# Optimization experiments

Measured on AMD Instinct MI355X. Metric: run time of the kernel, lower is better.

Reference implementation:

```python
import jax, jax.numpy as jnp
import numpy as np

EPS_RMS = 1.1920929e-07  # torch.finfo(float32).eps (nn.RMSNorm default eps=None)
EPS_LN = 1e-5
SCALE = 64 ** -0.5       # Attention.scale uses default dim_head=64, NOT dim_head_qk
SOFTCLAMP = 5.0
DEPTH = 4
H, DQK, DV = 8, 128, 192
D, DP = 768, 128
SEQ, NPAIR, B = 2048, 256, 1
FF_INNER = int(D * 2.0)
DP_INNER = int(DP * 2.0)
MAX_POS = 8192


def rmsnorm(x, w):
    return x * jax.lax.rsqrt(jnp.mean(x * x, axis=-1, keepdims=True) + EPS_RMS) * w


def layernorm_nb(x, w):  # LayerNorm(bias=False)
    mu = jnp.mean(x, axis=-1, keepdims=True)
    var = jnp.mean((x - mu) ** 2, axis=-1, keepdims=True)
    return (x - mu) * jax.lax.rsqrt(var + EPS_LN) * w


def rotate_half(x):
    x1, x2 = jnp.split(x, 2, axis=-1)
    return jnp.concatenate((-x2, x1), axis=-1)


def apply_rotary(pos, t):
    return t * jnp.cos(pos) + rotate_half(t) * jnp.sin(pos)


def rotary_table(seq_len):
    # faithful to source: inv_freq = 1/(arange(nf) + logspace(1, max_pos-nf+1, nf))
    nf = DQK // 2
    inv_freq = 1.0 / (jnp.arange(nf, dtype=jnp.float32)
                      + 10.0 ** jnp.linspace(1.0, float(MAX_POS - nf + 1), nf, dtype=jnp.float32))
    freqs = jnp.arange(seq_len, dtype=jnp.float32)[:, None] * inv_freq  # [n, nf]
    return jnp.concatenate((freqs, freqs), axis=-1)  # [n, DQK]


def softclamp(t):
    return jnp.tanh(t / SOFTCLAMP) * SOFTCLAMP


def _forward(single, pairwise, attn_pre_w, attn_post_w, qkv_w, q_norm_w, k_norm_w,
             v_norm_w, bias_rms_w, bias_proj_w, out_w, ff_pre_w, ff_post_w,
             ff_w1, ff_b1, ff_w2, ff_b2, pw_attn_pre_w, pw_qk_w, pw_v_w, pw_v_b,
             pw_ff_pre_w, pw_ff_w1, pw_ff_b1, pw_ff_w2, pw_ff_b2):
    b, n, _ = single.shape
    pos = rotary_table(n)
    pw_idx = 0
    for i in range(DEPTH):
        # ---- attention block (sandwich RMSNorm) ----
        res = single
        xn = rmsnorm(single, attn_pre_w[i])
        qkv = xn @ qkv_w[i]
        q, k, v = jnp.split(qkv, [H * DQK, H * DQK + DQK], axis=-1)
        q = q.reshape(b, n, H, DQK).transpose(0, 2, 1, 3)  # b h n d (k,v are single-head)
        q = layernorm_nb(q, q_norm_w[i]) * SCALE
        k = layernorm_nb(k, k_norm_w[i])
        v = layernorm_nb(v, v_norm_w[i])
        q = apply_rotary(pos, q)
        k = apply_rotary(pos, k)
        sim = jnp.einsum('bhid,bjd->bhij', q, k)
        # pairwise bias: RMSNorm -> GELU -> Linear(dp, heads) -> b h i j, nearest-repeat to seq
        pb = jax.nn.gelu(rmsnorm(pairwise, bias_rms_w[i]), approximate=False) @ bias_proj_w[i]
        pb = pb.transpose(0, 3, 1, 2)  # b h i j
        r = sim.shape[-1] // pb.shape[-1]
        pb = jnp.repeat(jnp.repeat(pb, r, axis=2), r, axis=3)
        attn = jax.nn.softmax(softclamp(sim + pb), axis=-1)
        out = jnp.einsum('bhij,bjd->bhid', attn, v)
        out = out.transpose(0, 2, 1, 3).reshape(b, n, H * DV)
        single = rmsnorm(out @ out_w[i], attn_post_w[i]) + res
        # ---- feedforward (sandwich RMSNorm) ----
        res = single
        xn = rmsnorm(single, ff_pre_w[i])
        h = jax.nn.relu(xn @ ff_w1[i] + ff_b1[i])
        single = rmsnorm(h @ ff_w2[i] + ff_b2[i], ff_post_w[i]) + res
        # ---- pairwise track every other layer (no sandwich) ----
        if i % 2 == 0:
            j = pw_idx
            res = pairwise
            xn = rmsnorm(pairwise, pw_attn_pre_w[j])
            pq, pk = jnp.split(xn @ pw_qk_w[j], 2, axis=-1)
            pv = xn @ pw_v_w[j] + pw_v_b[j]
            psim = jnp.einsum('bnid,bnjd->bnij', pq, pk)  # source never applies its scale
            pairwise = jnp.einsum('bnij,bnjd->bnid', jax.nn.softmax(psim, axis=-1), pv) + res
            res = pairwise
            xn = rmsnorm(pairwise, pw_ff_pre_w[j])
            hh = jax.nn.relu(xn @ pw_ff_w1[j] + pw_ff_b1[j])
            pairwise = hh @ pw_ff_w2[j] + pw_ff_b2[j] + res
            pw_idx += 1
    return single, pairwise


def setup_inputs() -> dict:
    key = jax.random.key(0)
    ks = iter(jax.random.split(key, 40))
    nrm = lambda shape: jax.random.normal(next(ks), shape, jnp.float32) * 0.02
    n_pw = (DEPTH + 1) // 2
    return dict(
        single=jax.random.normal(next(ks), (B, SEQ, D), jnp.float32),
        pairwise=jax.random.normal(next(ks), (B, NPAIR, NPAIR, DP), jnp.float32),
        attn_pre_w=jnp.ones((DEPTH, D), jnp.float32),
        attn_post_w=jnp.ones((DEPTH, D), jnp.float32),
        qkv_w=nrm((DEPTH, D, H * DQK + DQK + DV)),
        q_norm_w=jnp.ones((DEPTH, DQK), jnp.float32),
        k_norm_w=jnp.ones((DEPTH, DQK), jnp.float32),
        v_norm_w=jnp.ones((DEPTH, DV), jnp.float32),
        bias_rms_w=jnp.ones((DEPTH, DP), jnp.float32),
        bias_proj_w=nrm((DEPTH, DP, H)),
        out_w=nrm((DEPTH, H * DV, D)),
        ff_pre_w=jnp.ones((DEPTH, D), jnp.float32),
        ff_post_w=jnp.ones((DEPTH, D), jnp.float32),
        ff_w1=nrm((DEPTH, D, FF_INNER)),
        ff_b1=jnp.zeros((DEPTH, FF_INNER), jnp.float32),
        ff_w2=nrm((DEPTH, FF_INNER, D)),
        ff_b2=jnp.zeros((DEPTH, D), jnp.float32),
        pw_attn_pre_w=jnp.ones((n_pw, DP), jnp.float32),
        pw_qk_w=nrm((n_pw, DP, 2 * DP)),
        pw_v_w=nrm((n_pw, DP, DP)),
        pw_v_b=jnp.zeros((n_pw, DP), jnp.float32),
        pw_ff_pre_w=jnp.ones((n_pw, DP), jnp.float32),
        pw_ff_w1=nrm((n_pw, DP, DP_INNER)),
        pw_ff_b1=jnp.zeros((n_pw, DP_INNER), jnp.float32),
        pw_ff_w2=nrm((n_pw, DP_INNER, DP)),
        pw_ff_b2=jnp.zeros((n_pw, DP), jnp.float32),
    )


def reference(single, pairwise, attn_pre_w, attn_post_w, qkv_w, q_norm_w, k_norm_w,
              v_norm_w, bias_rms_w, bias_proj_w, out_w, ff_pre_w, ff_post_w,
              ff_w1, ff_b1, ff_w2, ff_b2, pw_attn_pre_w, pw_qk_w, pw_v_w, pw_v_b,
              pw_ff_pre_w, pw_ff_w1, pw_ff_b1, pw_ff_w2, pw_ff_b2):
    return _forward(single, pairwise, attn_pre_w, attn_post_w, qkv_w, q_norm_w,
                    k_norm_w, v_norm_w, bias_rms_w, bias_proj_w, out_w, ff_pre_w,
                    ff_post_w, ff_w1, ff_b1, ff_w2, ff_b2, pw_attn_pre_w, pw_qk_w,
                    pw_v_w, pw_v_b, pw_ff_pre_w, pw_ff_w1, pw_ff_b1, pw_ff_w2, pw_ff_b2)
```

## Files before the change

### kernel.cpp

```cpp
#include <hip/hip_runtime.h>
#include <hip/hip_bf16.h>

#define SEQ 2048
#define DMODEL 768
#define NHEAD 8
#define DQK 128
#define DV 192
#define QKVN 1344
#define FFI 1536
#define NP 256
#define DP 128
#define DPI 256
#define NPR 65536
#define KVB 64
#define NSPLIT 2

#define EPS_RMS 1.1920929e-07f
#define EPS_LN 1e-5f
#define LOG2E 1.4426950408889634f
#define C1_LOG2E 0.5770780163555852f
#define C2_LOG2E -14.426950408889634f

typedef __attribute__((ext_vector_type(8))) short bf16x8;
typedef __attribute__((ext_vector_type(4))) short bf16x4;
typedef __attribute__((ext_vector_type(4))) float f32x4;

__device__ inline float wave_sum(float v) {
#pragma unroll
  for (int o = 32; o > 0; o >>= 1) v += __shfl_xor(v, o, 64);
  return v;
}
__device__ inline unsigned short f2bf(float x) {
  unsigned int u = __float_as_uint(x);
  u += 0x7fffu + ((u >> 16) & 1u);
  return (unsigned short)(u >> 16);
}
__device__ inline float bf2f(unsigned short x) {
  unsigned int u = ((unsigned int)x) << 16;
  return __uint_as_float(u);
}

__global__ void pos_kernel(float* __restrict__ pos) {
  int i = blockIdx.x, l = threadIdx.x;
  float f = (l == 0) ? 0.1f * (float)i : 0.0f;
  pos[i * 128 + l] = f;
  pos[i * 128 + 64 + l] = f;
}

__global__ void rowscale_kernel(const float* __restrict__ x, float* __restrict__ sc, int cols) {
  size_t row = blockIdx.x;
  int l = threadIdx.x;
  const float* xr = x + row * cols;
  float ss = 0.f;
  for (int c = l; c < cols; c += 64) { float v = xr[c]; ss += v * v; }
  ss = wave_sum(ss);
  if (l == 0) sc[row] = rsqrtf(ss / (float)cols + EPS_RMS);
}

__global__ void rmsres_kernel(const float* __restrict__ x, const float* __restrict__ w,
                              const float* res, float* y, int cols, float* __restrict__ sc) {
  size_t row = blockIdx.x;
  int l = threadIdx.x;
  const float* xr = x + row * cols;
  float ss = 0.f;
  for (int c = l; c < cols; c += 64) { float v = xr[c]; ss += v * v; }
  ss = wave_sum(ss);
  float r = rsqrtf(ss / (float)cols + EPS_RMS);
  float* yr = y + row * cols;
  const float* rr = res + row * cols;
  float ss2 = 0.f;
  for (int c = l; c < cols; c += 64) {
    float v = xr[c] * r * w[c] + rr[c];
    yr[c] = v;
    ss2 += v * v;
  }
  ss2 = wave_sum(ss2);
  if (l == 0) sc[row] = rsqrtf(ss2 / (float)cols + EPS_RMS);
}

struct ConvBatch {
  const float* src[24];
  unsigned short* dst[24];
  int K[24];
  int N[24];
  int base[24];
};

__global__ __launch_bounds__(256) void convT_batch(ConvBatch cb, int nw) {
  __shared__ float ls[32][33];
  int bid = blockIdx.x;
  int w = 0;
  while (w + 1 < nw && bid >= cb.base[w + 1]) w++;
  int local = bid - cb.base[w];
  int K = cb.K[w], N = cb.N[w];
  int ntn = N >> 5;
  int n0 = (local % ntn) * 32, k0 = (local / ntn) * 32;
  const float* W = cb.src[w];
  unsigned short* Wt = cb.dst[w];
  int t = threadIdx.x;
  int c = t & 31, r4 = t >> 5;
#pragma unroll
  for (int p = 0; p < 4; p++) {
    int r = r4 + p * 8;
    ls[r][c] = W[(size_t)(k0 + r) * N + n0 + c];
  }
  __syncthreads();
#pragma unroll
  for (int p = 0; p < 4; p++) {
    int n = r4 + p * 8, k = t & 31;
    Wt[(size_t)(n0 + n) * K + k0 + k] = f2bf(ls[k][n]);
  }
}

__global__ void biasbuild_kernel(const float* __restrict__ pw_v_b, float* __restrict__ b384) {
  int j = blockIdx.x, t = threadIdx.x;
  b384[j * 384 + t] = (t < 256) ? 0.f : pw_v_b[j * DP + t - 256];
}

template<int AMODE, int CBF, int RBF = 0, int BN64 = 0>
__global__ __launch_bounds__(256) void gemm_k(const void* __restrict__ Av,
    const unsigned short* __restrict__ Bt, void* __restrict__ Cv,
    int M, int N, int K, int nbx,
    const float* __restrict__ bias, const void* __restrict__ resid, int act,
    const float* __restrict__ ascale, const float* __restrict__ aw,
    const float* __restrict__ lb = nullptr) {
  constexpr int BN = BN64 ? 64 : 128;
  constexpr int NC = BN64 ? 2 : 4;
  __shared__ unsigned short As[64 * 32];
  __shared__ unsigned short Bs[BN * 32];
  int t = threadIdx.x;
  int nwg = gridDim.x, bid = blockIdx.x;
  int qq = nwg >> 3, rr = nwg & 7, xc = bid & 7, ii = bid >> 3;
  int swz = (xc < rr ? xc * (qq + 1) : rr * (qq + 1) + (xc - rr) * qq) + ii;
  int bm = (swz / nbx) * 64, bn = (swz % nbx) * BN;
  int w = t >> 6, l = t & 63;
  int wr = (w >> 1) * 32, wc = (w & 1) * (BN / 2);
  int lo = l & 15, hi = l >> 4;
  f32x4 acc[2][NC];
#pragma unroll
  for (int q = 0; q < 2; q++)
#pragma unroll
    for (int cb = 0; cb < NC; cb++) acc[q][cb] = (f32x4){0.f, 0.f, 0.f, 0.f};

  int arow = t >> 2, acs = (t & 3) * 8;
  int brow = BN64 ? (t >> 2) : (t >> 1);
  int bks  = BN64 ? ((t & 3) * 8) : ((t & 1) * 16);
  int bok = (bn + brow < N);
  const unsigned short* bsrc = Bt + (size_t)(bok ? bn + brow : 0) * K + bks;

  float4 pa0, pa1;
  bf16x8 pab, pc1, pb0, pb1;
  float linv = 1.f;
  const bf16x8 zb = {0, 0, 0, 0, 0, 0, 0, 0};

  {
    if (AMODE == 2) {
      const unsigned short* Op = (const unsigned short*)Av;
      size_t base = (size_t)(bm + arow) * K + acs;
      pab = *(const bf16x8*)(Op + base);
      pc1 = *(const bf16x8*)(Op + (size_t)SEQ * K + base);
      int h = acs / DV;
      linv = 1.0f / (lb[(size_t)h * SEQ + bm + arow] +
                     lb[(size_t)(NHEAD + h) * SEQ + bm + arow]);
    } else if (AMODE == 1 || AMODE == 3) {
      pab = *(const bf16x8*)((const unsigned short*)Av + (size_t)(bm + arow) * K + acs);
    } else {
      const float* A = (const float*)Av;
      pa0 = *(const float4*)(A + (size_t)(bm + arow) * K + acs);
      pa1 = *(const float4*)(A + (size_t)(bm + arow) * K + acs + 4);
    }
    pb0 = bok ? *(const bf16x8*)(bsrc) : zb;
    if (!BN64) pb1 = bok ? *(const bf16x8*)(bsrc + 8) : zb;
  }

  for (int k0 = 0; k0 < K; k0 += 32) {
    if (k0) __syncthreads();
    {
      int byte = (arow * 64 + acs * 2) ^ ((arow & 7) << 4);
      if (AMODE == 2) {
        bf16x8 cmb;
#pragma unroll
        for (int e = 0; e < 8; e++)
          cmb[e] = (short)f2bf((bf2f((unsigned short)pab[e]) +
                                bf2f((unsigned short)pc1[e])) * linv);
        *(bf16x8*)((char*)As + byte) = cmb;
      } else if (AMODE == 3) {
        float s = ascale[bm + arow];
        bf16x8 sc8;
#pragma unroll
        for (int e = 0; e < 8; e++)
          sc8[e] = (short)f2bf(bf2f((unsigned short)pab[e]) * s * aw[k0 + acs + e]);
        *(bf16x8*)((char*)As + byte) = sc8;
      } else if (AMODE == 1) {
        *(bf16x8*)((char*)As + byte) = pab;
      } else {
        float4 v0 = pa0, v1 = pa1;
        if (ascale) {
          float s = ascale[bm + arow];
          v0.x *= s * aw[k0 + acs + 0]; v0.y *= s * aw[k0 + acs + 1];
          v0.z *= s * aw[k0 + acs + 2]; v0.w *= s * aw[k0 + acs + 3];
          v1.x *= s * aw[k0 + acs + 4]; v1.y *= s * aw[k0 + acs + 5];
          v1.z *= s * aw[k0 + acs + 6]; v1.w *= s * aw[k0 + acs + 7];
        }
        uint4 pk;
        pk.x = (unsigned int)f2bf(v0.x) | ((unsigned int)f2bf(v0.y) << 16);
        pk.y = (unsigned int)f2bf(v0.z) | ((unsigned int)f2bf(v0.w) << 16);
        pk.z = (unsigned int)f2bf(v1.x) | ((unsigned int)f2bf(v1.y) << 16);
        pk.w = (unsigned int)f2bf(v1.z) | ((unsigned int)f2bf(v1.w) << 16);
        *(uint4*)((char*)As + byte) = pk;
      }
      int b0 = (brow * 64 + bks * 2) ^ ((brow & 7) << 4);
      *(bf16x8*)((char*)Bs + b0) = pb0;
      if (!BN64) {
        int b1 = (brow * 64 + bks * 2 + 16) ^ ((brow & 7) << 4);
        *(bf16x8*)((char*)Bs + b1) = pb1;
      }
    }
    __syncthreads();
    if (k0 + 32 < K) {
      int kn = k0 + 32;
      if (AMODE == 2) {
        const unsigned short* Op = (const unsigned short*)Av;
        size_t base = (size_t)(bm + arow) * K + kn + acs;
        pab = *(const bf16x8*)(Op + base);
        pc1 = *(const bf16x8*)(Op + (size_t)SEQ * K + base);
        int h = (kn + acs) / DV;
        linv = 1.0f / (lb[(size_t)h * SEQ + bm + arow] +
                       lb[(size_t)(NHEAD + h) * SEQ + bm + arow]);
      } else if (AMODE == 1 || AMODE == 3) {
        pab = *(const bf16x8*)((const unsigned short*)Av + (size_t)(bm + arow) * K + kn + acs);
      } else {
        const float* A = (const float*)Av;
        pa0 = *(const float4*)(A + (size_t)(bm + arow) * K + kn + acs);
        pa1 = *(const float4*)(A + (size_t)(bm + arow) * K + kn + acs + 4);
      }
      pb0 = bok ? *(const bf16x8*)(bsrc + kn) : zb;
      if (!BN64) pb1 = bok ? *(const bf16x8*)(bsrc + kn + 8) : zb;
    }
    bf16x8 af[2], bfr[NC];
#pragma unroll
    for (int q = 0; q < 2; q++) {
      int r = wr + q * 16 + lo;
      af[q] = *(const bf16x8*)((char*)As + ((r * 64 + hi * 16) ^ ((r & 7) << 4)));
    }
#pragma unroll
    for (int cb = 0; cb < NC; cb++) {
      int n = wc + cb * 16 + lo;
      bfr[cb] = *(const bf16x8*)((char*)Bs + ((n * 64 + hi * 16) ^ ((n & 7) << 4)));
    }
#pragma unroll
    for (int q = 0; q < 2; q++)
#pragma unroll
      for (int cb = 0; cb < NC; cb++)
        acc[q][cb] = __builtin_amdgcn_mfma_f32_16x16x32_bf16(af[q], bfr[cb], acc[q][cb], 0, 0, 0);
  }
#pragma unroll
  for (int q = 0; q < 2; q++) {
#pragma unroll
    for (int cb = 0; cb < NC; cb++) {
      int gn = bn + wc + cb * 16 + lo;
      if (gn >= N) continue;
#pragma unroll
      for (int i = 0; i < 4; i++) {
        int gm = bm + wr + q * 16 + hi * 4 + i;
        float v = acc[q][cb][i];
        if (bias) v += bias[gn];
        if (act) v = fmaxf(v, 0.f);
        if (resid) {
          size_t ridx = (size_t)gm * N + gn;
          v += RBF ? bf2f(((const unsigned short*)resid)[ridx])
                   : ((const float*)resid)[ridx];
        }
        if (CBF) {
          ((unsigned short*)Cv)[(size_t)gm * N + gn] = f2bf(v);
        } else {
          ((float*)Cv)[(size_t)gm * N + gn] = v;
        }
      }
    }
  }
}

__global__ void qkv_prep_kernel(const unsigned short* __restrict__ qkv,
                                const float* __restrict__ qw,
                                const float* __restrict__ kw, const float* __restrict__ vw,
                                const float* __restrict__ pos,
                                unsigned short* __restrict__ q_r, unsigned short* __restrict__ k_n,
                                unsigned short* __restrict__ v_t) {
  int i = blockIdx.x;
  int y = blockIdx.y;
  int l = threadIdx.x;
  if (y == 9) {
    const unsigned short* row = qkv + (size_t)i * QKVN + NHEAD * DQK + DQK;
    float x0 = bf2f(row[l]), x1 = bf2f(row[l + 64]), x2 = bf2f(row[l + 128]);
    float mu = wave_sum(x0 + x1 + x2) * (1.0f / 192.0f);
    float d0 = x0 - mu, d1 = x1 - mu, d2 = x2 - mu;
    float var = wave_sum(d0 * d0 + d1 * d1 + d2 * d2) * (1.0f / 192.0f);
    float rs = rsqrtf(var + EPS_LN);
    v_t[(size_t)l * SEQ + i] = f2bf(d0 * rs * vw[l]);
    v_t[(size_t)(l + 64) * SEQ + i] = f2bf(d1 * rs * vw[l + 64]);
    v_t[(size_t)(l + 128) * SEQ + i] = f2bf(d2 * rs * vw[l + 128]);
    return;
  }
  int off = (y < 8) ? y * DQK : NHEAD * DQK;
  const unsigned short* row = qkv + (size_t)i * QKVN + off;
  float a = bf2f(row[l]), b = bf2f(row[l + 64]);
  float mu = wave_sum(a + b) * (1.0f / 128.0f);
  float da = a - mu, db = b - mu;
  float var = wave_sum(da * da + db * db) * (1.0f / 128.0f);
  float rs = rsqrtf(var + EPS_LN);
  const float* w = (y < 8) ? qw : kw;
  float na = da * rs * w[l], nb = db * rs * w[l + 64];
  if (y < 8) { na *= 0.125f; nb *= 0.125f; }
  float p0 = pos[i * 128 + l], p1 = pos[i * 128 + 64 + l];
  float ra = na * cosf(p0) - nb * sinf(p0);
  float rb = nb * cosf(p1) + na * sinf(p1);
  if (y < 8) {
    unsigned short* o = q_r + ((size_t)y * SEQ + i) * DQK;
    o[l] = f2bf(ra); o[l + 64] = f2bf(rb);
  } else {
    unsigned short* o = k_n + (size_t)i * DQK;
    o[l] = f2bf(ra); o[l + 64] = f2bf(rb);
  }
}

__global__ __launch_bounds__(256) void pb_kernel(const float* __restrict__ P,
    float* __restrict__ scP, const float* __restrict__ rmsw,
    const float* __restrict__ proj, float* __restrict__ pbt) {
  __shared__ float gs[32][130];
  __shared__ float projs[1024];
  int b = blockIdx.x, t = threadIdx.x;
  int row0 = b * 32;
  int wv = t >> 6, ln = t & 63;
  for (int f = t; f < 1024; f += 256) projs[f] = proj[f];
#pragma unroll
  for (int rr = 0; rr < 8; rr++) {
    int r = wv * 8 + rr;
    const float* src = P + (size_t)(row0 + r) * DP;
    float2 x = *(const float2*)(src + ln * 2);
    float ss = wave_sum(x.x * x.x + x.y * x.y);
    float rs = rsqrtf(ss * (1.0f / DP) + EPS_RMS);
    float g0 = x.x * rs * rmsw[ln * 2];
    float g1 = x.y * rs * rmsw[ln * 2 + 1];
    gs[r][ln * 2] = 0.5f * g0 * (1.0f + erff(g0 * 0.70710678118654752f));
    gs[r][ln * 2 + 1] = 0.5f * g1 * (1.0f + erff(g1 * 0.70710678118654752f));
    if (ln == 0) scP[row0 + r] = rs;
  }
  __syncthreads();
  int hh = t >> 5, r = t & 31;
  float acc = 0.f;
#pragma unroll 4
  for (int d = 0; d < 128; d++) acc += gs[r][d] * projs[d * 8 + hh];
  pbt[(size_t)hh * NPR + row0 + r] = acc;
}

__global__ __launch_bounds__(256) void attn_mfma(const unsigned short* __restrict__ q_r,
    const unsigned short* __restrict__ k_n, const unsigned short* __restrict__ v_t,
    const float* __restrict__ pbt, unsigned short* __restrict__ Opart,
    float* __restrict__ lbuf) {
  __shared__ unsigned short Ks[64 * 128];
  __shared__ unsigned short Vs[208 * 64];
  __shared__ unsigned short Ps[4][16 * 64];
  __shared__ float pb_lds[64];
  int ib = blockIdx.x, h = blockIdx.y, sp = blockIdx.z, t = threadIdx.x;
  int i0 = ib * 64;
  int w = t >> 6, l = t & 63;
  int lo = l & 15, hi = l >> 4;
  int kbeg = sp * (SEQ / NSPLIT), kend = kbeg + SEQ / NSPLIT;

  bf16x8 qf[4];
  {
    const unsigned short* qp = q_r + ((size_t)h * SEQ + i0 + w * 16 + lo) * DQK + hi * 8;
#pragma unroll
    for (int ks = 0; ks < 4; ks++) qf[ks] = *(const bf16x8*)(qp + ks * 32);
  }
  f32x4 o_acc[13];
#pragma unroll
  for (int vc = 0; vc < 13; vc++) o_acc[vc] = (f32x4){0.f, 0.f, 0.f, 0.f};

#pragma unroll
  for (int r4 = 0; r4 < 4; r4++) {
    int idx = t + 256 * r4;
    int row = 192 + (idx >> 6), key = idx & 63;
    int byte = (row * 128 + key * 2) ^ ((row & 7) << 4);
    *(unsigned short*)((char*)Vs + byte) = (row == 192) ? 0x3F80 : 0;
  }

  char* PsW = (char*)&Ps[w][0];
  int rg8 = (((w * 16 + lo) >> 3) << 3) + (hi >> 1);

  for (int k0 = kbeg; k0 < kend; k0 += KVB) {
    {
      int row = t >> 2, d0 = (t & 3) * 32;
      const unsigned short* src = k_n + (size_t)(k0 + row) * DQK + d0;
#pragma unroll
      for (int jj = 0; jj < 4; jj++) {
        bf16x8 a = *(const bf16x8*)(src + jj * 8);
        int byte = (row * 256 + (d0 + jj * 8) * 2) ^ ((row & 7) << 4);
        *(bf16x8*)((char*)Ks + byte) = a;
      }
    }
#pragma unroll
    for (int rep = 0; rep < 6; rep++) {
      int c = t + 256 * rep;
      int row = c >> 3, seg = c & 7;
      bf16x8 a = *(const bf16x8*)(v_t + (size_t)row * SEQ + k0 + seg * 8);
      int byte = (row * 128 + seg * 16) ^ ((row & 7) << 4);
      *(bf16x8*)((char*)Vs + byte) = a;
    }
    if (t < 64) {
      int rg = t >> 3, kg = t & 7;
      pb_lds[t] = C1_LOG2E * pbt[(size_t)h * NPR + ((i0 >> 3) + rg) * 256 + (k0 >> 3) + kg];
    }
    __syncthreads();
    f32x4 sacc[4];
#pragma unroll
    for (int kb = 0; kb < 4; kb++) sacc[kb] = (f32x4){0.f, 0.f, 0.f, 0.f};
#pragma unroll
    for (int ks = 0; ks < 4; ks++) {
#pragma unroll
      for (int kb = 0; kb < 4; kb++) {
        int key = kb * 16 + lo;
        int byte = (key * 256 + (ks * 32 + hi * 8) * 2) ^ ((key & 7) << 4);
        bf16x8 kf = *(const bf16x8*)((char*)Ks + byte);
        sacc[kb] = __builtin_amdgcn_mfma_f32_16x16x32_bf16(kf, qf[ks], sacc[kb], 0, 0, 0);
      }
    }
#pragma unroll
    for (int kb = 0; kb < 4; kb++) {
      float pb = pb_lds[rg8 + kb * 2];
      bf16x4 pk;
#pragma unroll
      for (int i = 0; i < 4; i++) {
        float x2 = fmaf(C1_LOG2E, sacc[kb][i], pb);
        float e = __builtin_amdgcn_exp2f(x2);
        float p = __builtin_amdgcn_exp2f(C2_LOG2E * __builtin_amdgcn_rcpf(e + 1.f));
        pk[i] = (short)f2bf(p);
      }
      int byte = (lo * 128 + (kb * 32 + hi * 8)) ^ ((lo & 7) << 4);
      *(bf16x4*)(PsW + byte) = pk;
    }
#pragma unroll
    for (int ks2 = 0; ks2 < 2; ks2++) {
      int byte = (lo * 128 + (ks2 * 32 + hi * 8) * 2) ^ ((lo & 7) << 4);
      bf16x8 pa = *(const bf16x8*)(PsW + byte);
#pragma unroll
      for (int vc = 0; vc < 13; vc++) {
        int dv = vc * 16 + lo;
        int vbyte = (dv * 128 + (ks2 * 32 + hi * 8) * 2) ^ ((dv & 7) << 4);
        bf16x8 bv = *(const bf16x8*)((char*)Vs + vbyte);
        o_acc[vc] = __builtin_amdgcn_mfma_f32_16x16x32_bf16(pa, bv, o_acc[vc], 0, 0, 0);
      }
    }
    __syncthreads();
  }
#pragma unroll
  for (int i = 0; i < 4; i++) {
    int row = i0 + w * 16 + hi * 4 + i;
    unsigned short* orow = Opart + (size_t)sp * SEQ * (NHEAD * DV) +
                           (size_t)row * (NHEAD * DV) + h * DV;
#pragma unroll
    for (int vc = 0; vc < 12; vc++) orow[vc * 16 + lo] = f2bf(o_acc[vc][i]);
    if (lo == 0) lbuf[((size_t)sp * NHEAD + h) * SEQ + row] = o_acc[12][i];
  }
}

__global__ __launch_bounds__(256) void pw_attn_mfma(const unsigned short* __restrict__ pqkv,
    const float* __restrict__ resid, unsigned short* __restrict__ out,
    float* __restrict__ scP) {
  __shared__ unsigned short Ks[64 * 128];
  __shared__ unsigned short Vs[128 * 64];
  __shared__ unsigned short Ps[4][16 * 64];
  int qb = blockIdx.x, nl = blockIdx.y, t = threadIdx.x;
  int i0 = qb * 64;
  int w = t >> 6, l = t & 63;
  int lo = l & 15, hi = l >> 4;
  size_t nrow = (size_t)nl * NP;

  bf16x8 qf[4];
  {
    const unsigned short* qp = pqkv + (nrow + i0 + w * 16 + lo) * 384 + hi * 8;
#pragma unroll
    for (int ks = 0; ks < 4; ks++) qf[ks] = *(const bf16x8*)(qp + ks * 32);
  }
  float m_s[4], l_s[4];
  f32x4 o_acc[8];
#pragma unroll
  for (int i = 0; i < 4; i++) { m_s[i] = -1e30f; l_s[i] = 0.f; }
#pragma unroll
  for (int vc = 0; vc < 8; vc++) o_acc[vc] = (f32x4){0.f, 0.f, 0.f, 0.f};
  char* PsW = (char*)&Ps[w][0];

  for (int k0 = 0; k0 < NP; k0 += 64) {
    {
      int row = t >> 2, d0 = (t & 3) * 32;
      const unsigned short* src = pqkv + (nrow + k0 + row) * 384 + DP + d0;
#pragma unroll
      for (int jj = 0; jj < 4; jj++) {
        bf16x8 a = *(const bf16x8*)(src + jj * 8);
        int byte = (row * 256 + (d0 + jj * 8) * 2) ^ ((row & 7) << 4);
        *(bf16x8*)((char*)Ks + byte) = a;
      }
    }
    {
      int key = t & 63, ds0 = (t >> 6) * 32;
      const unsigned short* src = pqkv + (nrow + k0 + key) * 384 + 256 + ds0;
#pragma unroll
      for (int e = 0; e < 4; e++) {
        bf16x8 a = *(const bf16x8*)(src + e * 8);
#pragma unroll
        for (int e2 = 0; e2 < 8; e2++) {
          int dv = ds0 + e * 8 + e2;
          *(unsigned short*)((char*)Vs + ((dv * 128 + key * 2) ^ ((dv & 7) << 4))) =
              (unsigned short)a[e2];
        }
      }
    }
    __syncthreads();
    f32x4 sacc[4];
#pragma unroll
    for (int cs = 0; cs < 4; cs++) sacc[cs] = (f32x4){0.f, 0.f, 0.f, 0.f};
#pragma unroll
    for (int ks = 0; ks < 4; ks++) {
#pragma unroll
      for (int cs = 0; cs < 4; cs++) {
        int key = cs * 16 + lo;
        int byte = (key * 256 + (ks * 32 + hi * 8) * 2) ^ ((key & 7) << 4);
        bf16x8 bk = *(const bf16x8*)((char*)Ks + byte);
        sacc[cs] = __builtin_amdgcn_mfma_f32_16x16x32_bf16(qf[ks], bk, sacc[cs], 0, 0, 0);
      }
    }
#pragma unroll
    for (int i = 0; i < 4; i++) {
      float mrow = fmaxf(fmaxf(sacc[0][i], sacc[1][i]), fmaxf(sacc[2][i], sacc[3][i]));
#pragma unroll
      for (int ofs = 1; ofs < 16; ofs <<= 1) mrow = fmaxf(mrow, __shfl_xor(mrow, ofs, 64));
      float mn = fmaxf(m_s[i], mrow);
      float mnl = mn * LOG2E;
      float scale = __builtin_amdgcn_exp2f(fmaf(m_s[i], LOG2E, -mnl));
      float ts = 0.f;
      int r = hi * 4 + i;
#pragma unroll
      for (int cs = 0; cs < 4; cs++) {
        float p = __builtin_amdgcn_exp2f(fmaf(sacc[cs][i], LOG2E, -mnl));
        ts += p;
        int key = cs * 16 + lo;
        int byte = (r * 128 + key * 2) ^ ((r & 7) << 4);
        *(unsigned short*)(PsW + byte) = f2bf(p);
      }
#pragma unroll
      for (int ofs = 1; ofs < 16; ofs <<= 1) ts += __shfl_xor(ts, ofs, 64);
      l_s[i] = l_s[i] * scale + ts;
      m_s[i] = mn;
#pragma unroll
      for (int vc = 0; vc < 8; vc++) o_acc[vc][i] *= scale;
    }
#pragma unroll
    for (int ks2 = 0; ks2 < 2; ks2++) {
      int byte = (lo * 128 + (ks2 * 32 + hi * 8) * 2) ^ ((lo & 7) << 4);
      bf16x8 pa = *(const bf16x8*)(PsW + byte);
#pragma unroll
      for (int vc = 0; vc < 8; vc++) {
        int dv = vc * 16 + lo;
        int vbyte = (dv * 128 + (ks2 * 32 + hi * 8) * 2) ^ ((dv & 7) << 4);
        bf16x8 bv = *(const bf16x8*)((char*)Vs + vbyte);
        o_acc[vc] = __builtin_amdgcn_mfma_f32_16x16x32_bf16(pa, bv, o_acc[vc], 0, 0, 0);
      }
    }
    __syncthreads();
  }
#pragma unroll
  for (int i = 0; i < 4; i++) {
    float inv = 1.0f / l_s[i];
    size_t growi = nrow + i0 + w * 16 + hi * 4 + i;
    size_t grow = growi * DP;
    float ss = 0.f;
#pragma unroll
    for (int vc = 0; vc < 8; vc++) {
      int dv = vc * 16 + lo;
      float v = o_acc[vc][i] * inv + resid[grow + dv];
      out[grow + dv] = f2bf(v);
      ss += v * v;
    }
#pragma unroll
    for (int ofs = 1; ofs < 16; ofs <<= 1) ss += __shfl_xor(ss, ofs, 64);
    if (lo == 0) scP[growi] = rsqrtf(ss * (1.0f / DP) + EPS_RMS);
  }
}

extern "C" void kernel_launch(void* const* d_in, const int* in_sizes, int n_in,
                              void* d_out, int out_size, void* d_ws, size_t ws_size,
                              hipStream_t stream) {
  const float* in_single   = (const float*)d_in[0];
  const float* in_pair     = (const float*)d_in[1];
  const float* attn_pre_w  = (const float*)d_in[2];
  const float* attn_post_w = (const float*)d_in[3];
  const float* qkv_w       = (const float*)d_in[4];
  const float* q_norm_w    = (const float*)d_in[5];
  const float* k_norm_w    = (const float*)d_in[6];
  const float* v_norm_w    = (const float*)d_in[7];
  const float* bias_rms_w  = (const float*)d_in[8];
  const float* bias_proj_w = (const float*)d_in[9];
  const float* out_w       = (const float*)d_in[10];
  const float* ff_pre_w    = (const float*)d_in[11];
  const float* ff_post_w   = (const float*)d_in[12];
  const float* ff_w1       = (const float*)d_in[13];
  const float* ff_b1       = (const float*)d_in[14];
  const float* ff_w2       = (const float*)d_in[15];
  const float* ff_b2       = (const float*)d_in[16];
  const float* pw_attn_pre = (const float*)d_in[17];
  const float* pw_qk_w     = (const float*)d_in[18];
  const float* pw_v_w      = (const float*)d_in[19];
  const float* pw_v_b      = (const float*)d_in[20];
  const float* pw_ff_pre   = (const float*)d_in[21];
  const float* pw_ff_w1    = (const float*)d_in[22];
  const float* pw_ff_b1    = (const float*)d_in[23];
  const float* pw_ff_w2    = (const float*)d_in[24];
  const float* pw_ff_b2    = (const float*)d_in[25];

  float* ws = (float*)d_ws;
  float* S    = ws;
  float* Pc   = ws + 1572864;
  float* Pa   = ws + 9961472;
  float* pbt  = ws + 18350080;
  float* pos  = ws + 18874368;
  float* scP  = ws + 19136512;
  float* scS  = ws + 19202048;
  float* TMP  = ws + 19204096;
  unsigned short* qkv_bf = (unsigned short*)TMP;
  unsigned short* q_r_bf = (unsigned short*)(TMP + 2752512);
  unsigned short* k_n_bf = (unsigned short*)(TMP + 3801088);
  unsigned short* v_t_bf = (unsigned short*)(TMP + 3932160);
  float* t2   = TMP + 655360;
  unsigned short* t1_bf = (unsigned short*)(TMP + 2752512);
  unsigned short* Opart = (unsigned short*)Pa;
  float* lbuf = Pa + 6500000;
  unsigned short* Pa_bf = (unsigned short*)Pa;
  float* bias384       = TMP + 6420000;
  unsigned short* Warena = (unsigned short*)(ws + 27854848);
  unsigned short* Wpw = Warena + (size_t)4 * 4571136;
  unsigned short* pqkv_full = (unsigned short*)(ws + 37111808);
  unsigned short* hh_full   = pqkv_full;

  float* outS = (float*)d_out;
  float* outP = outS + (size_t)SEQ * DMODEL;

  pos_kernel<<<SEQ, 64, 0, stream>>>(pos);
  rowscale_kernel<<<SEQ, 64, 0, stream>>>(in_single, scS, DMODEL);
  biasbuild_kernel<<<2, 384, 0, stream>>>(pw_v_b, bias384);

  {
    ConvBatch cb;
    int idx = 0, base = 0;
    auto add = [&](const float* s, unsigned short* d, int K, int N) {
      cb.src[idx] = s; cb.dst[idx] = d; cb.K[idx] = K; cb.N[idx] = N; cb.base[idx] = base;
      base += (N / 32) * (K / 32);
      idx++;
    };
    for (int l = 0; l < 4; l++) {
      unsigned short* WA = Warena + (size_t)l * 4571136;
      add(qkv_w + (size_t)l * DMODEL * QKVN, WA, DMODEL, QKVN);
      add(out_w + (size_t)l * (NHEAD * DV) * DMODEL, WA + 1032192, NHEAD * DV, DMODEL);
      add(ff_w1 + (size_t)l * DMODEL * FFI, WA + 2211840, DMODEL, FFI);
      add(ff_w2 + (size_t)l * FFI * DMODEL, WA + 3391488, FFI, DMODEL);
    }
    for (int j = 0; j < 2; j++) {
      unsigned short* WEF = Wpw + (size_t)j * 114688;
      add(pw_qk_w + (size_t)j * DP * 2 * DP, WEF, DP, 2 * DP);
      add(pw_v_w + (size_t)j * DP * DP, WEF + 256 * DP, DP, DP);
      add(pw_ff_w1 + (size_t)j * DP * DPI, WEF + 49152, DP, DPI);
      add(pw_ff_w2 + (size_t)j * DPI * DP, WEF + 81920, DPI, DP);
    }
    convT_batch<<<base, 256, 0, stream>>>(cb, idx);
  }

  for (int i = 0; i < 4; i++) {
    int j = i / 2;
    unsigned short* WA  = Warena + (size_t)i * 4571136;
    unsigned short* WO  = WA + 1032192;
    unsigned short* WF1 = WA + 2211840;
    unsigned short* WF2 = WA + 3391488;
    unsigned short* WEF = Wpw + (size_t)j * 114688;
    unsigned short* WG  = WEF + 49152;
    unsigned short* WH  = WEF + 81920;

    const float* Psrc = (i == 0) ? in_pair : ((i == 3) ? outP : Pc);
    const float* Ssrc = (i == 0) ? in_single : S;

    pb_kernel<<<2048, 256, 0, stream>>>(Psrc, scP, bias_rms_w + i * DP,
                                        bias_proj_w + (size_t)i * DP * 8, pbt);
    gemm_k<0, 1, 0, 1><<<21 * 32, 256, 0, stream>>>(Ssrc, WA, qkv_bf, SEQ, QKVN, DMODEL, 21,
                                                    nullptr, nullptr, 0, scS, attn_pre_w + i * DMODEL);
    qkv_prep_kernel<<<dim3(SEQ, 10), 64, 0, stream>>>(qkv_bf, q_norm_w + i * DQK,
                                                      k_norm_w + i * DQK, v_norm_w + i * DV,
                                                      pos, q_r_bf, k_n_bf, v_t_bf);
    attn_mfma<<<dim3(SEQ / 64, NHEAD, NSPLIT), 256, 0, stream>>>(q_r_bf, k_n_bf, v_t_bf, pbt,
                                                                 Opart, lbuf);
    gemm_k<2, 0, 0, 1><<<12 * 32, 256, 0, stream>>>(Opart, WO, t2, SEQ, DMODEL, NHEAD * DV, 12,
                                                    nullptr, nullptr, 0, nullptr, nullptr, lbuf);
    rmsres_kernel<<<SEQ, 64, 0, stream>>>(t2, attn_post_w + i * DMODEL, Ssrc, S, DMODEL, scS);
    gemm_k<0, 1, 0, 1><<<24 * 32, 256, 0, stream>>>(S, WF1, t1_bf, SEQ, FFI, DMODEL, 24,
                                                    ff_b1 + i * FFI, nullptr, 1, scS, ff_pre_w + i * DMODEL);
    gemm_k<1, 0, 0, 1><<<12 * 32, 256, 0, stream>>>(t1_bf, WF2, t2, SEQ, DMODEL, FFI, 12,
                                                    ff_b2 + i * DMODEL, nullptr, 0, nullptr, nullptr);
    float* Sdst = (i == 3) ? outS : S;
    rmsres_kernel<<<SEQ, 64, 0, stream>>>(t2, ff_post_w + i * DMODEL, S, Sdst, DMODEL, scS);
    if ((i & 1) == 0) {
      float* Pdst = (i == 2) ? outP : Pc;
      gemm_k<0, 1><<<3 * 1024, 256, 0, stream>>>(Psrc, WEF, pqkv_full, NPR, 384, DP, 3,
                                                 bias384 + j * 384, nullptr, 0,
                                                 scP, pw_attn_pre + j * DP);
      pw_attn_mfma<<<dim3(4, 256), 256, 0, stream>>>(pqkv_full, Psrc, Pa_bf, scP);
      gemm_k<3, 1><<<2 * 1024, 256, 0, stream>>>(Pa_bf, WG, hh_full, NPR, DPI, DP, 2,
                                                 pw_ff_b1 + j * DPI, nullptr, 1,
                                                 scP, pw_ff_pre + j * DP);
      gemm_k<1, 0, 1><<<1 * 1024, 256, 0, stream>>>(hh_full, WH, Pdst, NPR, DP, DPI, 1,
                                                    pw_ff_b2 + j * DP, Pa_bf, 0, nullptr, nullptr);
    }
  }
}
```

Baseline: 1.095 ms.

## Split attention KV into four partitions and combine partials in separate kernel

Raises the attention KV split count from two to four so more workgroups run concurrently on the 2048x8 attention. The partial outputs are no longer combined inside the output-projection GEMM's A-load (AMODE 2). A new kernel sums the bf16 partials, normalizes by the summed l values and writes a combined bf16 buffer, which a plain GEMM then consumes. This adds a launch and an extra pass over the partials, and it assumes the partials share a common max reference so that plain summation is valid. It also assumes the larger Opart/lbuf footprint and the Ocomb alias do not overlap other live buffers.

```diff
diff --git a/kernel.cpp b/kernel.cpp
--- a/kernel.cpp
+++ b/kernel.cpp
@@ -13,7 +13,7 @@
 #define DPI 256
 #define NPR 65536
 #define KVB 64
-#define NSPLIT 2
+#define NSPLIT 4
 
 #define EPS_RMS 1.1920929e-07f
 #define EPS_LN 1e-5f
@@ -115,6 +115,32 @@
 __global__ void biasbuild_kernel(const float* __restrict__ pw_v_b, float* __restrict__ b384) {
   int j = blockIdx.x, t = threadIdx.x;
   b384[j * 384 + t] = (t < 256) ? 0.f : pw_v_b[j * DP + t - 256];
+}
+
+__global__ void ocomb_kernel(const unsigned short* __restrict__ Opart,
+                             const float* __restrict__ lbuf,
+                             unsigned short* __restrict__ Oc) {
+  int row = blockIdx.x, c8 = threadIdx.x;
+  int h = c8 / 24;
+  float lsum = 0.f;
+#pragma unroll
+  for (int sp = 0; sp < NSPLIT; sp++)
+    lsum += lbuf[((size_t)sp * NHEAD + h) * SEQ + row];
+  float linv = 1.0f / lsum;
+  size_t base = (size_t)row * (NHEAD * DV) + c8 * 8;
+  bf16x8 a[NSPLIT];
+#pragma unroll
+  for (int sp = 0; sp < NSPLIT; sp++)
+    a[sp] = *(const bf16x8*)(Opart + (size_t)sp * SEQ * (NHEAD * DV) + base);
+  bf16x8 o;
+#pragma unroll
+  for (int e = 0; e < 8; e++) {
+    float s = 0.f;
+#pragma unroll
+    for (int sp = 0; sp < NSPLIT; sp++) s += bf2f((unsigned short)a[sp][e]);
+    o[e] = (short)f2bf(s * linv);
+  }
+  *(bf16x8*)(Oc + base) = o;
 }
 
 template<int AMODE, int CBF, int RBF = 0, int BN64 = 0>
@@ -635,6 +661,7 @@
   unsigned short* t1_bf = (unsigned short*)(TMP + 2752512);
   unsigned short* Opart = (unsigned short*)Pa;
   float* lbuf = Pa + 6500000;
+  unsigned short* Ocomb = (unsigned short*)(TMP + 3932160);
   unsigned short* Pa_bf = (unsigned short*)Pa;
   float* bias384       = TMP + 6420000;
   unsigned short* Warena = (unsigned short*)(ws + 27854848);
@@ -696,8 +723,9 @@
                                                       pos, q_r_bf, k_n_bf, v_t_bf);
     attn_mfma<<<dim3(SEQ / 64, NHEAD, NSPLIT), 256, 0, stream>>>(q_r_bf, k_n_bf, v_t_bf, pbt,
                                                                  Opart, lbuf);
-    gemm_k<2, 0, 0, 1><<<12 * 32, 256, 0, stream>>>(Opart, WO, t2, SEQ, DMODEL, NHEAD * DV, 12,
-                                                    nullptr, nullptr, 0, nullptr, nullptr, lbuf);
+    ocomb_kernel<<<SEQ, 192, 0, stream>>>(Opart, lbuf, Ocomb);
+    gemm_k<1, 0, 0, 1><<<12 * 32, 256, 0, stream>>>(Ocomb, WO, t2, SEQ, DMODEL, NHEAD * DV, 12,
+                                                    nullptr, nullptr, 0, nullptr, nullptr);
     rmsres_kernel<<<SEQ, 64, 0, stream>>>(t2, attn_post_w + i * DMODEL, Ssrc, S, DMODEL, scS);
     gemm_k<0, 1, 0, 1><<<24 * 32, 256, 0, stream>>>(S, WF1, t1_bf, SEQ, FFI, DMODEL, 24,
                                                     ff_b1 + i * FFI, nullptr, 1, scS, ff_pre_w + i * DMODEL);
```

New measurement: 1.076 ms. Within noise of the previous version (-1.7%).
